# Kernel optimization log

Measured on AMD Instinct MI355X. Metric: run time of the kernel, lower is better.

The kernel has to match this reference:

```python
import jax, jax.numpy as jnp
import numpy as np

N0 = 4096
C = 128
DEPTH = 3
RATIO = 0.5
AVG_DEG = 32
BN_EPS = 1e-5


def setup_inputs() -> dict:
    key = jax.random.key(0)
    ks = jax.random.split(key, 6)
    x = jax.random.normal(ks[0], (N0, C), dtype=jnp.float32)
    # sparse symmetric adjacency (avg degree ~AVG_DEG), no self loops, dense layout
    mask = jax.random.bernoulli(ks[1], AVG_DEG / N0, (N0, N0)).astype(jnp.float32)
    adj = jnp.maximum(mask, mask.T) * (1.0 - jnp.eye(N0, dtype=jnp.float32))
    scale = 1.0 / np.sqrt(C)
    conv_w = jax.random.normal(ks[2], (2 * DEPTH + 1, C, C), dtype=jnp.float32) * scale
    conv_b = jax.random.normal(ks[3], (2 * DEPTH + 1, C), dtype=jnp.float32) * 0.01
    pool_w = jax.random.normal(ks[4], (DEPTH, C), dtype=jnp.float32)
    bn_g = jnp.ones((2 * DEPTH + 1, C), dtype=jnp.float32)
    bn_b = jnp.zeros((2 * DEPTH + 1, C), dtype=jnp.float32)
    return {"x": x, "adj": adj, "conv_w": conv_w, "conv_b": conv_b,
            "pool_w": pool_w, "bn_g": bn_g, "bn_b": bn_b}


def _gcn(x, A, W, b):
    # GCNConv(improved=True): A_hat = A + 2I, symmetric deg normalization
    n = A.shape[0]
    Ah = A + 2.0 * jnp.eye(n, dtype=A.dtype)
    deg = Ah.sum(axis=1)
    d_safe = jnp.where(deg > 0, deg, 1.0)
    dn = jnp.where(deg > 0, jax.lax.rsqrt(d_safe), 0.0)
    An = dn[:, None] * Ah * dn[None, :]
    return An @ (x @ W) + b


def _bn(x, g, b):
    # BatchNorm1d, training mode (biased variance)
    m = x.mean(axis=0)
    v = x.var(axis=0)
    return g * (x - m) * jax.lax.rsqrt(v + BN_EPS) + b


def _augment(A):
    # add_self_loops -> spspmm(A,A) -> remove_self_loops, done densely
    n = A.shape[0]
    I = jnp.eye(n, dtype=A.dtype)
    Aa = A + I
    return (Aa @ Aa) * (1.0 - I)


def _topk_pool(x, A, p):
    score = jnp.tanh((x @ p) / jnp.linalg.norm(p))
    k = int(np.ceil(RATIO * x.shape[0]))
    vals, perm = jax.lax.top_k(score, k)
    xn = x[perm] * vals[:, None]
    An = A[perm][:, perm]
    return xn, An, perm


def reference(x, adj, conv_w, conv_b, pool_w, bn_g, bn_b):
    x = x.astype(jnp.float32)
    x = _bn(jax.nn.relu(_gcn(x, adj, conv_w[0], conv_b[0])), bn_g[0], bn_b[0])
    xs, adjs, perms = [x], [adj], []
    A = adj
    for i in range(1, DEPTH + 1):
        A2 = _augment(A)
        x, A, perm = _topk_pool(x, A2, pool_w[i - 1])
        x = _bn(jax.nn.relu(_gcn(x, A, conv_w[i], conv_b[i])), bn_g[i], bn_b[i])
        if i < DEPTH:
            xs.append(x)
            adjs.append(A)
        perms.append(perm)
    for i in range(DEPTH):
        j = DEPTH - 1 - i
        res, Aj, perm = xs[j], adjs[j], perms[j]
        up = jnp.zeros_like(res).at[perm].set(x)
        x = res + up  # sum_res=True
        x = _gcn(x, Aj, conv_w[DEPTH + 1 + i], conv_b[DEPTH + 1 + i])
        if i < DEPTH - 1:
            x = jax.nn.relu(x)
        x = _bn(x, bn_g[DEPTH + 1 + i], bn_b[DEPTH + 1 + i])
    return x
```

## Files before the change

kernel.cpp:

```cpp
#include <hip/hip_runtime.h>
#include <cstdint>
#include <cstddef>

typedef __bf16 bf16;
typedef __bf16 bf16x8 __attribute__((ext_vector_type(8)));
typedef __bf16 bf16x4 __attribute__((ext_vector_type(4)));
typedef float floatx4 __attribute__((ext_vector_type(4)));
typedef int   intx4  __attribute__((ext_vector_type(4)));
typedef short shortx4 __attribute__((ext_vector_type(4)));
typedef char  cx8    __attribute__((ext_vector_type(8)));

#define GLD16(gp, lp) __builtin_amdgcn_global_load_lds( \
    (const __attribute__((address_space(1))) void*)(gp), \
    (__attribute__((address_space(3))) void*)(lp), 16, 0, 0)

#define FXS 16777216.0f
#define FXI 5.9604644775390625e-08

__global__ __launch_bounds__(256) void gemm_sym_i8(
    const char* __restrict__ R, short* __restrict__ Cs16, int* __restrict__ Cs32,
    int n , int kIters, int G, int pairs)
{
  __shared__ __align__(16) char As[128 * 64];
  __shared__ __align__(16) char Bs[128 * 64];

  const int pair = blockIdx.x;
  int rem = pair, bm = 0;
  while (rem >= G - bm) { rem -= G - bm; ++bm; }
  const int bn = bm + rem;
  const int m0 = bm * 128;
  const int n0 = bn * 128;

  const int t = threadIdx.x;
  const int w = t >> 6, l = t & 63;
  const int wr = w >> 1, wc = w & 1;
  const int lr = l & 15, q = l >> 4;
  const int k0base = blockIdx.y * kIters * 64;

  const char* Ab = R + (size_t)m0 * n + k0base;
  const char* Bb = R + (size_t)n0 * n + k0base;
  const int srow = t >> 2;
  const int schunk = (t & 3) * 16;

  intx4 acc[4][4];
#pragma unroll
  for (int i = 0; i < 4; ++i)
#pragma unroll
    for (int j = 0; j < 4; ++j) acc[i][j] = (intx4)0;

  for (int kb = 0; kb < kIters; ++kb) {
    const int k0 = kb * 64;
    __syncthreads();
    GLD16(Ab + (size_t)srow * n + k0 + schunk,        As + (size_t)t * 16);
    GLD16(Ab + (size_t)(srow + 64) * n + k0 + schunk, As + (size_t)(t + 256) * 16);
    GLD16(Bb + (size_t)srow * n + k0 + schunk,        Bs + (size_t)t * 16);
    GLD16(Bb + (size_t)(srow + 64) * n + k0 + schunk, Bs + (size_t)(t + 256) * 16);
    __syncthreads();

    intx4 af[4], bfr[4];
#pragma unroll
    for (int mi = 0; mi < 4; ++mi)
      af[mi] = *(const intx4*)&As[(wr * 64 + mi * 16 + lr) * 64 + q * 16];
#pragma unroll
    for (int ni = 0; ni < 4; ++ni)
      bfr[ni] = *(const intx4*)&Bs[(wc * 64 + ni * 16 + lr) * 64 + q * 16];
#pragma unroll
    for (int mi = 0; mi < 4; ++mi)
#pragma unroll
      for (int ni = 0; ni < 4; ++ni)
        acc[mi][ni] = __builtin_amdgcn_mfma_i32_16x16x64_i8(
            af[mi], bfr[ni], acc[mi][ni], 0, 0, 0);
  }

  const size_t so = ((size_t)blockIdx.y * pairs + pair) * 16384;
#pragma unroll
  for (int mi = 0; mi < 4; ++mi)
#pragma unroll
    for (int ni = 0; ni < 4; ++ni) {
      const int cl = wc * 64 + ni * 16 + lr;
      const int rb = wr * 64 + mi * 16 + q * 4;
#pragma unroll
      for (int r = 0; r < 4; ++r) {
        int v = acc[mi][ni][r];
        if (Cs16) Cs16[so + (size_t)(rb + r) * 128 + cl] = (short)v;
        else      Cs32[so + (size_t)(rb + r) * 128 + cl] = v;
      }
    }
}

__global__ void sym_post_i(const short* __restrict__ Cs16, const int* __restrict__ Cs32,
                           bf16* __restrict__ Abf, float* __restrict__ Af,
                           int k, int G, int pairs, int nz)
{
  int rem = blockIdx.x, bm = 0;
  while (rem >= G - bm) { rem -= G - bm; ++bm; }
  const int bn = bm + rem;
  const int t = threadIdx.x;
  const int i = t >> 1;
  const int jc = blockIdx.y * 8 + (t & 1) * 4;
  const int r = bm * 128 + i;
  const size_t sbase = (size_t)blockIdx.x * 16384 + (size_t)i * 128 + jc;

  int v[4] = {0, 0, 0, 0};
  for (int z = 0; z < nz; ++z) {
    const size_t off = sbase + (size_t)z * pairs * 16384;
    if (Cs16) {
      shortx4 a = *(const shortx4*)&Cs16[off];
#pragma unroll
      for (int e = 0; e < 4; ++e) v[e] += (int)a[e];
    } else {
      intx4 a = *(const intx4*)&Cs32[off];
#pragma unroll
      for (int e = 0; e < 4; ++e) v[e] += a[e];
    }
  }
  const int c0 = bn * 128 + jc;
#pragma unroll
  for (int e = 0; e < 4; ++e)
    if (c0 + e == r) v[e] = 0;

  if (Abf) {
    bf16x4 o;
#pragma unroll
    for (int e = 0; e < 4; ++e) o[e] = (bf16)(float)v[e];
    *(bf16x4*)&Abf[(size_t)r * k + c0] = o;
    if (bm != bn) {
#pragma unroll
      for (int e = 0; e < 4; ++e)
        Abf[(size_t)(c0 + e) * k + r] = o[e];
    }
  } else {
    floatx4 o;
#pragma unroll
    for (int e = 0; e < 4; ++e) o[e] = (float)v[e];
    *(floatx4*)&Af[(size_t)r * k + c0] = o;
    if (bm != bn) {
#pragma unroll
      for (int e = 0; e < 4; ++e)
        Af[(size_t)(c0 + e) * k + r] = o[e];
    }
  }
}

__global__ __launch_bounds__(256) void gemm_sym(
    const bf16* __restrict__ R, float* __restrict__ CsF,
    int n , int kIters, int G, int pairs)
{
  __shared__ __align__(16) bf16 As[128 * 32];
  __shared__ __align__(16) bf16 Bs[128 * 32];

  const int pair = blockIdx.x;
  int rem = pair, bm = 0;
  while (rem >= G - bm) { rem -= G - bm; ++bm; }
  const int bn = bm + rem;
  const int m0 = bm * 128;
  const int n0 = bn * 128;

  const int t = threadIdx.x;
  const int w = t >> 6, l = t & 63;
  const int wr = w >> 1, wc = w & 1;
  const int lr = l & 15, q = l >> 4;
  const int k0base = blockIdx.y * kIters * 32;

  const bf16* Ab = R + (size_t)m0 * n + k0base;
  const bf16* Bb = R + (size_t)n0 * n + k0base;
  const int srow = t >> 2;
  const int schunk = (t & 3) * 8;

  floatx4 acc[4][4];
#pragma unroll
  for (int i = 0; i < 4; ++i)
#pragma unroll
    for (int j = 0; j < 4; ++j) acc[i][j] = (floatx4)0.0f;

  for (int kb = 0; kb < kIters; ++kb) {
    const int k0 = kb * 32;
    __syncthreads();
    GLD16(Ab + (size_t)srow * n + k0 + schunk,        As + (size_t)t * 8);
    GLD16(Ab + (size_t)(srow + 64) * n + k0 + schunk, As + (size_t)(t + 256) * 8);
    GLD16(Bb + (size_t)srow * n + k0 + schunk,        Bs + (size_t)t * 8);
    GLD16(Bb + (size_t)(srow + 64) * n + k0 + schunk, Bs + (size_t)(t + 256) * 8);
    __syncthreads();

    bf16x8 af[4], bfr[4];
#pragma unroll
    for (int mi = 0; mi < 4; ++mi)
      af[mi] = *(const bf16x8*)&As[(wr * 64 + mi * 16 + lr) * 32 + q * 8];
#pragma unroll
    for (int ni = 0; ni < 4; ++ni)
      bfr[ni] = *(const bf16x8*)&Bs[(wc * 64 + ni * 16 + lr) * 32 + q * 8];
#pragma unroll
    for (int mi = 0; mi < 4; ++mi)
#pragma unroll
      for (int ni = 0; ni < 4; ++ni)
        acc[mi][ni] = __builtin_amdgcn_mfma_f32_16x16x32_bf16(
            af[mi], bfr[ni], acc[mi][ni], 0, 0, 0);
  }

  const size_t so = ((size_t)blockIdx.y * pairs + pair) * 16384;
#pragma unroll
  for (int mi = 0; mi < 4; ++mi)
#pragma unroll
    for (int ni = 0; ni < 4; ++ni) {
      const int cl = wc * 64 + ni * 16 + lr;
      const int rb = wr * 64 + mi * 16 + q * 4;
#pragma unroll
      for (int r = 0; r < 4; ++r)
        CsF[so + (size_t)(rb + r) * 128 + cl] = acc[mi][ni][r];
    }
}

__global__ void sym_post(const float* __restrict__ CsF, float* __restrict__ Af,
                         int k, int G, int pairs, int nz)
{
  int rem = blockIdx.x, bm = 0;
  while (rem >= G - bm) { rem -= G - bm; ++bm; }
  const int bn = bm + rem;
  const int t = threadIdx.x;
  const int i = t >> 1;
  const int jc = blockIdx.y * 8 + (t & 1) * 4;
  const int r = bm * 128 + i;
  const size_t sbase = (size_t)blockIdx.x * 16384 + (size_t)i * 128 + jc;

  float v[4] = {0.f, 0.f, 0.f, 0.f};
  for (int z = 0; z < nz; ++z) {
    const size_t off = sbase + (size_t)z * pairs * 16384;
    floatx4 a = *(const floatx4*)&CsF[off];
#pragma unroll
    for (int e = 0; e < 4; ++e) v[e] += a[e];
  }
  const int c0 = bn * 128 + jc;
  floatx4 o;
#pragma unroll
  for (int e = 0; e < 4; ++e) o[e] = (c0 + e == r) ? 0.0f : v[e];
  *(floatx4*)&Af[(size_t)r * k + c0] = o;
  if (bm != bn) {
#pragma unroll
    for (int e = 0; e < 4; ++e)
      Af[(size_t)(c0 + e) * k + r] = o[e];
  }
}

__global__ __launch_bounds__(256) void agg_sparse(
    const unsigned short* __restrict__ nbr, const int* __restrict__ deg,
    const float* __restrict__ Z, float* __restrict__ Y)
{
  const int r = blockIdx.x * 4 + (threadIdx.x >> 6);
  const int l = threadIdx.x & 63;
  const unsigned short* rn = nbr + (size_t)r * 256;
  const int d = deg[r];
  float a0 = 0.f, a1 = 0.f;
  int i = 0;
  for (; i + 4 <= d; i += 4) {
    const int c0 = rn[i], c1 = rn[i + 1], c2 = rn[i + 2], c3 = rn[i + 3];
    float2 v0 = *(const float2*)(Z + (size_t)c0 * 128 + l * 2);
    float2 v1 = *(const float2*)(Z + (size_t)c1 * 128 + l * 2);
    float2 v2 = *(const float2*)(Z + (size_t)c2 * 128 + l * 2);
    float2 v3 = *(const float2*)(Z + (size_t)c3 * 128 + l * 2);
    a0 += v0.x; a1 += v0.y;
    a0 += v1.x; a1 += v1.y;
    a0 += v2.x; a1 += v2.y;
    a0 += v3.x; a1 += v3.y;
  }
  for (; i < d; ++i) {
    const int c = rn[i];
    float2 v = *(const float2*)(Z + (size_t)c * 128 + l * 2);
    a0 += v.x; a1 += v.y;
  }
  *(float2*)(Y + (size_t)r * 128 + l * 2) = make_float2(a0, a1);
}

template <int NP>
__global__ __launch_bounds__(256) void agg_bf(
    const bf16* __restrict__ A, int lda,
    const bf16* __restrict__ Zh, const bf16* __restrict__ Zm, const bf16* __restrict__ Zl,
    int ldz, float* __restrict__ Y, int kIters)
{
  __shared__ __align__(16) bf16 As[64 * 32];
  __shared__ __align__(16) bf16 Zs[NP][128 * 32];

  const int t = threadIdx.x;
  const int w = t >> 6, l = t & 63;
  const int wr = w >> 1, wc = w & 1;
  const int lr = l & 15, q = l >> 4;
  const int m0 = blockIdx.x * 64;
  const int k0base = blockIdx.y * kIters * 32;

  const int srow = t >> 2;
  const int schunk = (t & 3) * 8;

  floatx4 acc[2][4];
#pragma unroll
  for (int i = 0; i < 2; ++i)
#pragma unroll
    for (int j = 0; j < 4; ++j) acc[i][j] = (floatx4)0.0f;

  for (int kb = 0; kb < kIters; ++kb) {
    const int k0 = k0base + kb * 32;
    __syncthreads();
    GLD16(A + (size_t)(m0 + srow) * lda + k0 + schunk, As + (size_t)t * 8);
    GLD16(Zh + (size_t)srow * ldz + k0 + schunk,        Zs[0] + (size_t)t * 8);
    GLD16(Zh + (size_t)(srow + 64) * ldz + k0 + schunk, Zs[0] + (size_t)(t + 256) * 8);
    GLD16(Zm + (size_t)srow * ldz + k0 + schunk,        Zs[1] + (size_t)t * 8);
    GLD16(Zm + (size_t)(srow + 64) * ldz + k0 + schunk, Zs[1] + (size_t)(t + 256) * 8);
    if (NP > 2) {
      GLD16(Zl + (size_t)srow * ldz + k0 + schunk,        Zs[2] + (size_t)t * 8);
      GLD16(Zl + (size_t)(srow + 64) * ldz + k0 + schunk, Zs[2] + (size_t)(t + 256) * 8);
    }
    __syncthreads();

    bf16x8 af[2], bz[NP][4];
#pragma unroll
    for (int mi = 0; mi < 2; ++mi)
      af[mi] = *(const bf16x8*)&As[(wr * 32 + mi * 16 + lr) * 32 + q * 8];
#pragma unroll
    for (int s = 0; s < NP; ++s)
#pragma unroll
      for (int ni = 0; ni < 4; ++ni)
        bz[s][ni] = *(const bf16x8*)&Zs[s][(wc * 64 + ni * 16 + lr) * 32 + q * 8];
#pragma unroll
    for (int s = 0; s < NP; ++s)
#pragma unroll
      for (int mi = 0; mi < 2; ++mi)
#pragma unroll
        for (int ni = 0; ni < 4; ++ni)
          acc[mi][ni] = __builtin_amdgcn_mfma_f32_16x16x32_bf16(
              af[mi], bz[s][ni], acc[mi][ni], 0, 0, 0);
  }

  const size_t zoff = (size_t)blockIdx.y * lda;
#pragma unroll
  for (int mi = 0; mi < 2; ++mi)
#pragma unroll
    for (int ni = 0; ni < 4; ++ni) {
      const int col = wc * 64 + ni * 16 + lr;
      const int rowb = m0 + wr * 32 + mi * 16 + q * 4;
#pragma unroll
      for (int r = 0; r < 4; ++r)
        Y[(zoff + rowb + r) * 128 + col] = acc[mi][ni][r];
    }
}

template <int NP>
__global__ __launch_bounds__(256) void agg_split(
    const float* __restrict__ A, int lda,
    const bf16* __restrict__ Zh, const bf16* __restrict__ Zm, const bf16* __restrict__ Zl,
    int ldz, float* __restrict__ Y, int kIters, int aTwo)
{
  __shared__ __align__(16) bf16 Ahs[64 * 32];
  __shared__ __align__(16) bf16 Als[64 * 32];
  __shared__ __align__(16) bf16 Zs[NP][128 * 32];

  const int t = threadIdx.x;
  const int w = t >> 6, l = t & 63;
  const int wr = w >> 1, wc = w & 1;
  const int lr = l & 15, q = l >> 4;
  const int m0 = blockIdx.x * 64;
  const int k0base = blockIdx.y * kIters * 32;

  const int arow = t >> 2;
  const int acol = (t & 3) * 8;
  const int srow = t >> 2;
  const int schunk = (t & 3) * 8;

  floatx4 acc[2][4];
#pragma unroll
  for (int i = 0; i < 2; ++i)
#pragma unroll
    for (int j = 0; j < 4; ++j) acc[i][j] = (floatx4)0.0f;

  for (int kb = 0; kb < kIters; ++kb) {
    const int k0 = k0base + kb * 32;
    const float* asrc = A + (size_t)(m0 + arow) * lda + k0 + acol;
    floatx4 av[2];
#pragma unroll
    for (int i = 0; i < 2; ++i) av[i] = *(const floatx4*)(asrc + i * 4);

    __syncthreads();
    GLD16(Zh + (size_t)srow * ldz + k0 + schunk,        Zs[0] + (size_t)t * 8);
    GLD16(Zh + (size_t)(srow + 64) * ldz + k0 + schunk, Zs[0] + (size_t)(t + 256) * 8);
    GLD16(Zm + (size_t)srow * ldz + k0 + schunk,        Zs[1] + (size_t)t * 8);
    GLD16(Zm + (size_t)(srow + 64) * ldz + k0 + schunk, Zs[1] + (size_t)(t + 256) * 8);
    if (NP > 2) {
      GLD16(Zl + (size_t)srow * ldz + k0 + schunk,        Zs[2] + (size_t)t * 8);
      GLD16(Zl + (size_t)(srow + 64) * ldz + k0 + schunk, Zs[2] + (size_t)(t + 256) * 8);
    }

    bf16x4 ah[2], alo[2];
    const int grow = m0 + arow;
#pragma unroll
    for (int i = 0; i < 8; ++i) {
      float v = av[i >> 2][i & 3];
      if (k0 + acol + i == grow) v = 0.0f;
      bf16 h = (bf16)v;
      ah[i >> 2][i & 3] = h;
      alo[i >> 2][i & 3] = (bf16)(v - (float)h);
    }
    const int sbase = arow * 32 + acol;
    *(bf16x4*)&Ahs[sbase] = ah[0]; *(bf16x4*)&Ahs[sbase + 4] = ah[1];
    if (aTwo) { *(bf16x4*)&Als[sbase] = alo[0]; *(bf16x4*)&Als[sbase + 4] = alo[1]; }
    __syncthreads();

    bf16x8 afh[2], afl[2], bz[NP][4];
#pragma unroll
    for (int mi = 0; mi < 2; ++mi)
      afh[mi] = *(const bf16x8*)&Ahs[(wr * 32 + mi * 16 + lr) * 32 + q * 8];
#pragma unroll
    for (int s = 0; s < NP; ++s)
#pragma unroll
      for (int ni = 0; ni < 4; ++ni)
        bz[s][ni] = *(const bf16x8*)&Zs[s][(wc * 64 + ni * 16 + lr) * 32 + q * 8];
#pragma unroll
    for (int s = 0; s < NP; ++s)
#pragma unroll
      for (int mi = 0; mi < 2; ++mi)
#pragma unroll
        for (int ni = 0; ni < 4; ++ni)
          acc[mi][ni] = __builtin_amdgcn_mfma_f32_16x16x32_bf16(
              afh[mi], bz[s][ni], acc[mi][ni], 0, 0, 0);
    if (aTwo) {
#pragma unroll
      for (int mi = 0; mi < 2; ++mi)
        afl[mi] = *(const bf16x8*)&Als[(wr * 32 + mi * 16 + lr) * 32 + q * 8];
      constexpr int NL = (NP > 2) ? 2 : 1;
#pragma unroll
      for (int s = 0; s < NL; ++s)
#pragma unroll
        for (int mi = 0; mi < 2; ++mi)
#pragma unroll
          for (int ni = 0; ni < 4; ++ni)
            acc[mi][ni] = __builtin_amdgcn_mfma_f32_16x16x32_bf16(
                afl[mi], bz[s][ni], acc[mi][ni], 0, 0, 0);
    }
  }

  const size_t zoff = (size_t)blockIdx.y * lda;
#pragma unroll
  for (int mi = 0; mi < 2; ++mi)
#pragma unroll
    for (int ni = 0; ni < 4; ++ni) {
      const int col = wc * 64 + ni * 16 + lr;
      const int rowb = m0 + wr * 32 + mi * 16 + q * 4;
#pragma unroll
      for (int r = 0; r < 4; ++r)
        Y[(zoff + rowb + r) * 128 + col] = acc[mi][ni][r];
    }
}

template <int FULL>
__global__ __launch_bounds__(256) void xw_split(
    const float* __restrict__ X, const int* __restrict__ perm,
    const float* __restrict__ vals,
    const float* __restrict__ up, const int* __restrict__ inv,
    const long long* __restrict__ statsP, const float* __restrict__ gP,
    const float* __restrict__ bP, float nP,
    const bf16* __restrict__ Wh, const bf16* __restrict__ Wm, const bf16* __restrict__ Wl,
    const float* __restrict__ dnv, float* __restrict__ Z,
    bf16* __restrict__ Zht, bf16* __restrict__ Zmt, bf16* __restrict__ Zlt, int ldz,
    long long* __restrict__ stats)
{
  __shared__ __align__(16) bf16 Xs[3][128 * 32];
  __shared__ __align__(16) bf16 Ws[3][128 * 32];
  __shared__ float scU[128], offU[128];

  const int t = threadIdx.x;
  if (blockIdx.x == 0) stats[t] = 0;

  const int w = t >> 6, l = t & 63;
  const int wr = w >> 1, wc = w & 1;
  const int lr = l & 15, q = l >> 4;
  const int r0 = blockIdx.x * 128;

  const int srow = t >> 1;
  const int soff = (t & 1) * 16;
  const int sbase = srow * 32 + soff;

  if (statsP) {
    if (t < 128) {
      float sm = (float)((double)statsP[t] * FXI);
      float sq = (float)((double)statsP[128 + t] * FXI);
      float m = sm / nP;
      float var = sq / nP - m * m;
      float sc = gP[t] / sqrtf(var + 1e-5f);
      scU[t] = sc;
      offU[t] = bP[t] - m * sc;
    }
    __syncthreads();
  }

  const int row = r0 + srow;
  int grow = row;
  float scale = 1.0f;
  if (perm) { grow = perm[row]; scale = vals[row]; }
  const float* xrow = X + (size_t)grow * 128;
  const float* uprow = nullptr;
  if (up) { int j = inv[row]; if (j >= 0) uprow = up + (size_t)j * 128; }

  floatx4 acc[4][4];
#pragma unroll
  for (int i = 0; i < 4; ++i)
#pragma unroll
    for (int j = 0; j < 4; ++j) acc[i][j] = (floatx4)0.0f;

  const bf16* wsrc[3] = {Wh, Wm, Wl};

  for (int ks = 0; ks < 4; ++ks) {
    const int k0 = ks * 32;
    float xv[16];
#pragma unroll
    for (int i = 0; i < 16; i += 4) {
      floatx4 tmp = *(const floatx4*)(xrow + k0 + soff + i);
      if (uprow) {
        floatx4 u = *(const floatx4*)(uprow + k0 + soff + i);
        if (statsP) {
#pragma unroll
          for (int j = 0; j < 4; ++j) {
            const int c = k0 + soff + i + j;
            u[j] = scU[c] * u[j] + offU[c];
          }
        }
        tmp += u;
      }
      xv[i] = tmp[0] * scale; xv[i + 1] = tmp[1] * scale;
      xv[i + 2] = tmp[2] * scale; xv[i + 3] = tmp[3] * scale;
    }
    bf16x8 wv[3][2];
#pragma unroll
    for (int s = 0; s < 3; ++s) {
      const bf16* ws = wsrc[s] + (size_t)srow * 128 + k0 + soff;
      wv[s][0] = *(const bf16x8*)ws;
      wv[s][1] = *(const bf16x8*)(ws + 8);
    }
    bf16x8 vh[2], vm[2], vl[2];
#pragma unroll
    for (int i = 0; i < 16; ++i) {
      float v = xv[i];
      bf16 h = (bf16)v; float r1 = v - (float)h;
      bf16 m = (bf16)r1; float r2 = r1 - (float)m;
      vh[i >> 3][i & 7] = h; vm[i >> 3][i & 7] = m; vl[i >> 3][i & 7] = (bf16)r2;
    }
    __syncthreads();
    *(bf16x8*)&Xs[0][sbase] = vh[0]; *(bf16x8*)&Xs[0][sbase + 8] = vh[1];
    *(bf16x8*)&Xs[1][sbase] = vm[0]; *(bf16x8*)&Xs[1][sbase + 8] = vm[1];
    *(bf16x8*)&Xs[2][sbase] = vl[0]; *(bf16x8*)&Xs[2][sbase + 8] = vl[1];
#pragma unroll
    for (int s = 0; s < 3; ++s) {
      *(bf16x8*)&Ws[s][sbase] = wv[s][0];
      *(bf16x8*)&Ws[s][sbase + 8] = wv[s][1];
    }
    __syncthreads();

    bf16x8 af[3][4], bfg[3][4];
#pragma unroll
    for (int s = 0; s < 3; ++s) {
#pragma unroll
      for (int mi = 0; mi < 4; ++mi)
        af[s][mi] = *(const bf16x8*)&Xs[s][(wr * 64 + mi * 16 + lr) * 32 + q * 8];
#pragma unroll
      for (int ni = 0; ni < 4; ++ni)
        bfg[s][ni] = *(const bf16x8*)&Ws[s][(wc * 64 + ni * 16 + lr) * 32 + q * 8];
    }
    constexpr int NT = FULL ? 6 : 3;
    constexpr int sa[6] = {0, 0, 1, 1, 0, 2};
    constexpr int sb[6] = {0, 1, 0, 1, 2, 0};
#pragma unroll
    for (int p = 0; p < NT; ++p)
#pragma unroll
      for (int mi = 0; mi < 4; ++mi)
#pragma unroll
        for (int ni = 0; ni < 4; ++ni)
          acc[mi][ni] = __builtin_amdgcn_mfma_f32_16x16x32_bf16(
              af[sa[p]][mi], bfg[sb[p]][ni], acc[mi][ni], 0, 0, 0);
  }

#pragma unroll
  for (int mi = 0; mi < 4; ++mi) {
    const int rowb = r0 + wr * 64 + mi * 16 + q * 4;
    float dnr[4];
#pragma unroll
    for (int r = 0; r < 4; ++r) dnr[r] = dnv[rowb + r];
#pragma unroll
    for (int ni = 0; ni < 4; ++ni) {
      const int col = wc * 64 + ni * 16 + lr;
      bf16x4 h4, m4, l4;
#pragma unroll
      for (int r = 0; r < 4; ++r) {
        float v = dnr[r] * acc[mi][ni][r];
        Z[(size_t)(rowb + r) * 128 + col] = v;
        bf16 h = (bf16)v; float r1 = v - (float)h;
        bf16 m = (bf16)r1; float r2 = r1 - (float)m;
        h4[r] = h; m4[r] = m; l4[r] = (bf16)r2;
      }
      if (Zht) {
        *(bf16x4*)&Zht[(size_t)col * ldz + rowb] = h4;
        *(bf16x4*)&Zmt[(size_t)col * ldz + rowb] = m4;
        if (FULL) *(bf16x4*)&Zlt[(size_t)col * ldz + rowb] = l4;
      }
    }
  }
}

__global__ void prep_all(const float* __restrict__ adj, bf16* __restrict__ ah,
                         float* __restrict__ dn, int n,
                         unsigned short* __restrict__ nbr, int* __restrict__ deg,
                         const float* __restrict__ W, bf16* __restrict__ Wh,
                         bf16* __restrict__ Wm, bf16* __restrict__ Wl,
                         const float* __restrict__ pw, float* __restrict__ invp) {
  const int bid = blockIdx.x;
  const int t = threadIdx.x;
  __shared__ int wsum4[4];
  __shared__ float red[128];
  if (bid < 4096) {
    const int r = bid;
    const float* arow = adj + (size_t)r * n;
    bf16* orow = ah + (size_t)r * n;
    const int base = t * 16;
    floatx4 buf[4];
#pragma unroll
    for (int i = 0; i < 4; ++i) buf[i] = *(const floatx4*)(arow + base + i * 4);
    int cnt = 0;
#pragma unroll
    for (int i = 0; i < 4; ++i) {
      bf16x4 o;
#pragma unroll
      for (int e = 0; e < 4; ++e) {
        float x = (base + i * 4 + e == r) ? 0.0f : buf[i][e];
        buf[i][e] = x;
        cnt += (x != 0.0f) ? 1 : 0;
        o[e] = (bf16)x;
      }
      *(bf16x4*)&orow[base + i * 4] = o;
    }
    const int lane = t & 63, wid = t >> 6;
    int vc = cnt;
#pragma unroll
    for (int off = 1; off < 64; off <<= 1) {
      int u = __shfl_up(vc, off, 64);
      if (lane >= off) vc += u;
    }
    if (lane == 63) wsum4[wid] = vc;
    __syncthreads();
    int add = 0;
    for (int wi = 0; wi < wid; ++wi) add += wsum4[wi];
    int o = vc + add - cnt;
    const int total = wsum4[0] + wsum4[1] + wsum4[2] + wsum4[3];
    unsigned short* rn = nbr + (size_t)r * 256;
#pragma unroll
    for (int i = 0; i < 4; ++i)
#pragma unroll
      for (int e = 0; e < 4; ++e)
        if (buf[i][e] != 0.0f) {
          if (o < 256) rn[o] = (unsigned short)(base + i * 4 + e);
          ++o;
        }
    if (t == 0) {
      deg[r] = total < 256 ? total : 256;
      dn[r] = 1.0f / sqrtf((float)total + 2.0f);
    }
  } else if (bid < 4544) {
    int idx = (bid - 4096) * 256 + t;
    int l = idx >> 14, rem = idx & 16383, c = rem >> 7, k = rem & 127;
    float v = W[(l << 14) + (k << 7) + c];
    bf16 h = (bf16)v; float r1 = v - (float)h;
    bf16 m = (bf16)r1; float r2 = r1 - (float)m;
    Wh[idx] = h; Wm[idx] = m; Wl[idx] = (bf16)r2;
  } else {
    if (t < 128) {
      for (int l = 0; l < 3; ++l) {
        float v = pw[l * 128 + t];
        red[t] = v * v; __syncthreads();
        for (int off = 64; off; off >>= 1) {
          if (t < off) red[t] += red[t + off];
          __syncthreads();
        }
        if (t == 0) invp[l] = 1.0f / sqrtf(red[0]);
        __syncthreads();
      }
    }
  }
}

__global__ void dn_rows_bf(const bf16* __restrict__ A, int lda, float* __restrict__ dn,
                           int n) {
  int r = blockIdx.x, t = threadIdx.x;
  const bf16* row = A + (size_t)r * lda;
  float sum = 0.f;
  for (int c4 = t * 4; c4 < n; c4 += 1024) {
    bf16x4 v = *(const bf16x4*)&row[c4];
#pragma unroll
    for (int e = 0; e < 4; ++e) sum += (float)v[e];
  }
  __shared__ float red[256];
  red[t] = sum; __syncthreads();
  for (int off = 128; off; off >>= 1) {
    if (t < off) red[t] += red[t + off];
    __syncthreads();
  }
  if (t == 0) dn[r] = 1.0f / sqrtf(red[0] + 2.0f);
}

__global__ void dn_rows(const float* __restrict__ A, int lda, float* __restrict__ dn,
                        int n) {
  int r = blockIdx.x, t = threadIdx.x;
  const float* row = A + (size_t)r * lda;
  float sum = 0.f;
  for (int c = t; c < n; c += 256)
    if (c != r) sum += row[c];
  __shared__ float red[256];
  red[t] = sum; __syncthreads();
  for (int off = 128; off; off >>= 1) {
    if (t < off) red[t] += red[t + off];
    __syncthreads();
  }
  if (t == 0) dn[r] = 1.0f / sqrtf(red[0] + 2.0f);
}

__device__ inline unsigned f2u(float f) {
  unsigned u = __float_as_uint(f);
  return (u & 0x80000000u) ? ~u : (u | 0x80000000u);
}
__global__ __launch_bounds__(1024) void select_kernel(
    const float* __restrict__ s, int n, int k,
    int* __restrict__ perm, float* __restrict__ vals, int* __restrict__ inv)
{
  __shared__ int hist[256];
  __shared__ unsigned sh_prefix;
  __shared__ int sh_krem;
  __shared__ float sh_thr;
  __shared__ int wsum[16];
  __shared__ int wgs[16], wes[16];
  const int t = threadIdx.x;
  const int lane = t & 63;
  const int wid = t >> 6;
  if (t == 0) { sh_prefix = 0; sh_krem = k; }

  for (int round = 0; round < 4; ++round) {
    const int shift = 24 - 8 * round;
    if (t < 256) hist[t] = 0;
    __syncthreads();
    const unsigned pref = sh_prefix;
    const int krem = sh_krem;
    for (int i = t; i < n; i += 1024) {
      unsigned u = f2u(s[i]);
      if (round == 0 || (u >> (shift + 8)) == pref)
        atomicAdd(&hist[(u >> shift) & 255], 1);
    }
    __syncthreads();
    int v = 0, own = 0;
    if (t < 256) {
      own = hist[255 - t];
      v = own;
#pragma unroll
      for (int off = 1; off < 64; off <<= 1) {
        int u = __shfl_up(v, off, 64);
        if (lane >= off) v += u;
      }
      if (lane == 63) wsum[wid] = v;
    }
    __syncthreads();
    if (t < 256) {
      int add = 0;
      for (int wi = 0; wi < wid; ++wi) add += wsum[wi];
      v += add;
      const int prev = v - own;
      if (v >= krem && prev < krem) {
        sh_prefix = (pref << 8) | (unsigned)(255 - t);
        sh_krem = krem - prev;
      }
    }
    __syncthreads();
  }
  if (t == 0) {
    unsigned u = sh_prefix;
    sh_thr = (u & 0x80000000u) ? __uint_as_float(u & 0x7fffffffu)
                               : __uint_as_float(~u);
  }
  for (int i = t; i < n; i += 1024) inv[i] = -1;
  __syncthreads();

  const float thr = sh_thr;
  const int chunk = n >> 10;
  const int beg = t * chunk;
  int g = 0, e = 0;
  for (int i = 0; i < chunk; ++i) {
    float v = s[beg + i];
    g += (v > thr); e += (v == thr);
  }
  int vg = g, ve = e;
#pragma unroll
  for (int off = 1; off < 64; off <<= 1) {
    int ug = __shfl_up(vg, off, 64);
    int ue = __shfl_up(ve, off, 64);
    if (lane >= off) { vg += ug; ve += ue; }
  }
  if (lane == 63) { wgs[wid] = vg; wes[wid] = ve; }
  __syncthreads();
  int ag = 0, ae = 0;
  for (int wi = 0; wi < wid; ++wi) { ag += wgs[wi]; ae += wes[wi]; }
  int total_gt = 0;
#pragma unroll
  for (int wi = 0; wi < 16; ++wi) total_gt += wgs[wi];
  int pg = vg + ag - g;
  int pe = ve + ae - e;
  const int need = k - total_gt;
  for (int i = 0; i < chunk; ++i) {
    float v = s[beg + i];
    if (v > thr) {
      if (pg < k) { perm[pg] = beg + i; vals[pg] = v; inv[beg + i] = pg; }
      ++pg;
    } else if (v == thr) {
      if (pe < need && total_gt + pe < k) {
        perm[total_gt + pe] = beg + i; vals[total_gt + pe] = v;
        inv[beg + i] = total_gt + pe;
      }
      ++pe;
    }
  }
}

__global__ void gather_i8(const bf16* __restrict__ src, int lda,
                          const int* __restrict__ perm, char* __restrict__ R, int n) {
  int j = blockIdx.x, t = threadIdx.x;
  int r = perm[j];
  const bf16* s = src + (size_t)r * lda;
  char* o = R + (size_t)j * n;
  for (int c = t * 8; c < n; c += 2048) {
    bf16x8 v = *(const bf16x8*)&s[c];
    cx8 ob;
#pragma unroll
    for (int e = 0; e < 8; ++e)
      ob[e] = (c + e == r) ? (char)1 : (char)(float)v[e];
    *(cx8*)&o[c] = ob;
  }
}

__global__ void gather_f32(const float* __restrict__ src, int lda,
                           const int* __restrict__ perm, bf16* __restrict__ R, int n) {
  int j = blockIdx.x, t = threadIdx.x;
  int r = perm[j];
  const float* s = src + (size_t)r * lda;
  bf16* o = R + (size_t)j * n;
  for (int c4 = t * 4; c4 < n; c4 += 1024) {
    floatx4 v = *(const floatx4*)(s + c4);
    bf16x4 ob;
#pragma unroll
    for (int e = 0; e < 4; ++e)
      ob[e] = (c4 + e == r) ? (bf16)1.0f : (bf16)v[e];
    *(bf16x4*)&o[c4] = ob;
  }
}

__global__ void gcn_post(const float* Ys, const float* __restrict__ Zf,
                         const float* __restrict__ dn, const float* __restrict__ bias,
                         long long* __restrict__ stats, int relu,
                         float* hout, int nr, int nz) {
  int c = threadIdx.x;
  int r0 = blockIdx.x * 4;
  float b = bias[c];
  float s = 0.f, qq = 0.f;
  for (int i = 0; i < 4; ++i) {
    int r = r0 + i;
    float a = 0.f;
    for (int z = 0; z < nz; ++z)
      a += Ys[((size_t)z * nr + r) * 128 + c];
    float v = dn[r] * (a + 2.0f * Zf[(size_t)r * 128 + c]) + b;
    if (relu) v = fmaxf(v, 0.f);
    hout[(size_t)r * 128 + c] = v;
    s += v; qq += v * v;
  }
  atomicAdd((unsigned long long*)&stats[c],
            (unsigned long long)(long long)llrintf(s * FXS));
  atomicAdd((unsigned long long*)&stats[128 + c],
            (unsigned long long)(long long)llrintf(qq * FXS));
}

__global__ void bn_apply(const float* __restrict__ H, const long long* __restrict__ stats,
                         const float* __restrict__ g, const float* __restrict__ b,
                         int n, float* __restrict__ xout,
                         const float* __restrict__ pw, const float* __restrict__ invp,
                         float* __restrict__ scores) {
  int r = blockIdx.x, c = threadIdx.x;
  float sm = (float)((double)stats[c] * FXI);
  float sq = (float)((double)stats[128 + c] * FXI);
  float m = sm / n;
  float var = sq / n - m * m;
  float sc = g[c] / sqrtf(var + 1e-5f);
  float off = b[c] - m * sc;
  float v = sc * H[(size_t)r * 128 + c] + off;
  xout[(size_t)r * 128 + c] = v;
  if (pw) {
    __shared__ float red[128];
    red[c] = v * pw[c]; __syncthreads();
    for (int o = 64; o; o >>= 1) {
      if (c < o) red[c] += red[c + o];
      __syncthreads();
    }
    if (c == 0) scores[r] = tanhf(red[0] * invp[0]);
  }
}

extern "C" void kernel_launch(void* const* d_in, const int* in_sizes, int n_in,
                              void* d_out, int out_size, void* d_ws, size_t ws_size,
                              hipStream_t stream) {
  const float* x_in   = (const float*)d_in[0];
  const float* adj    = (const float*)d_in[1];
  const float* conv_w = (const float*)d_in[2];
  const float* conv_b = (const float*)d_in[3];
  const float* pool_w = (const float*)d_in[4];
  const float* bn_g   = (const float*)d_in[5];
  const float* bn_b   = (const float*)d_in[6];
  float* out = (float*)d_out;
  (void)in_sizes; (void)n_in; (void)out_size; (void)ws_size;

  char* p = (char*)d_ws;
  auto alloc = [&](size_t bytes) -> void* {
    void* r = (void*)p;
    p += (bytes + 255) & ~(size_t)255;
    return r;
  };
  bf16*  Ah0bf = (bf16*)alloc(4096ull * 4096 * 2);
  bf16*  A1bf  = (bf16*)alloc(2048ull * 2048 * 2);
  float* A2f   = (float*)alloc(1024ull * 1024 * 4);
  float* A3f   = (float*)alloc(512ull * 512 * 4);
  char*  Rbuf  = (char*)alloc(2048ull * 4096 * 2);
  void*  Cs    = alloc(40ull << 20);
  float* Z     = (float*)alloc(4096ull * 128 * 4);
  bf16*  Zht   = (bf16*)alloc(128ull * 4096 * 2);
  bf16*  Zmt   = (bf16*)alloc(128ull * 4096 * 2);
  bf16*  Zlt   = (bf16*)alloc(128ull * 4096 * 2);
  float* Agg   = (float*)alloc(8ull * 2048 * 128 * 4);
  float* res0  = (float*)alloc(4096ull * 128 * 4);
  float* res1  = (float*)alloc(2048ull * 128 * 4);
  float* res2  = (float*)alloc(1024ull * 128 * 4);
  float* xb0   = (float*)alloc(512ull * 128 * 4);
  float* xb1   = (float*)alloc(1024ull * 128 * 4);
  float* xb2   = (float*)alloc(2048ull * 128 * 4);
  bf16*  Wh    = (bf16*)alloc(7ull * 16384 * 2);
  bf16*  Wm    = (bf16*)alloc(7ull * 16384 * 2);
  bf16*  Wl    = (bf16*)alloc(7ull * 16384 * 2);
  unsigned short* nbr = (unsigned short*)alloc(4096ull * 256 * 2 + 1024);
  int*   deg   = (int*)alloc(4096 * 4);
  float* scores = (float*)alloc(4096 * 4);
  int*   perm0 = (int*)alloc(2048 * 4);
  int*   perm1 = (int*)alloc(1024 * 4);
  int*   perm2 = (int*)alloc(512 * 4);
  int*   inv0  = (int*)alloc(4096 * 4);
  int*   inv1  = (int*)alloc(2048 * 4);
  int*   inv2  = (int*)alloc(1024 * 4);
  float* vals0 = (float*)alloc(2048 * 4);
  float* vals1 = (float*)alloc(1024 * 4);
  float* vals2 = (float*)alloc(512 * 4);
  float* dn0   = (float*)alloc(4096 * 4);
  float* dn1   = (float*)alloc(2048 * 4);
  float* dn2   = (float*)alloc(1024 * 4);
  float* dn3   = (float*)alloc(512 * 4);
  float* invp  = (float*)alloc(256);
  long long* stats = (long long*)alloc(7ull * 256 * 8);

  auto gcn = [&](int nr, const bf16* Abf, const float* Af32,
                 const unsigned short* nbrp, const float* dnv,
                 int layer, const float* xsrc, const int* perm, const float* vals,
                 const float* up, const int* inv, float* xout, int relu, int aTwo,
                 const float* pw, const float* ip, int full,
                 const long long* statsP, const float* gP, const float* bPv, float nP,
                 int doBn) {
    long long* st = stats + layer * 256;
    bf16* zht = nbrp ? nullptr : Zht;
    bf16* zmt = nbrp ? nullptr : Zmt;
    bf16* zlt = nbrp ? nullptr : Zlt;
    if (full)
      xw_split<1><<<nr / 128, 256, 0, stream>>>(
          xsrc, perm, vals, up, inv, statsP, gP, bPv, nP,
          Wh + layer * 16384, Wm + layer * 16384, Wl + layer * 16384, dnv,
          Z, zht, zmt, zlt, nr, st);
    else
      xw_split<0><<<nr / 128, 256, 0, stream>>>(
          xsrc, perm, vals, up, inv, statsP, gP, bPv, nP,
          Wh + layer * 16384, Wm + layer * 16384, Wl + layer * 16384, dnv,
          Z, zht, zmt, zlt, nr, st);
    int nz;
    if (nbrp) {
      agg_sparse<<<nr / 4, 256, 0, stream>>>(nbrp, deg, Z, Agg);
      nz = 1;
    } else if (Abf) {
      if (full)
        agg_bf<3><<<dim3(nr / 64, 8), 256, 0, stream>>>(
            Abf, nr, Zht, Zmt, Zlt, nr, Agg, nr / 256);
      else
        agg_bf<2><<<dim3(nr / 64, 8), 256, 0, stream>>>(
            Abf, nr, Zht, Zmt, Zlt, nr, Agg, nr / 256);
      nz = 8;
    } else {
      if (full)
        agg_split<3><<<dim3(nr / 64, 8), 256, 0, stream>>>(
            Af32, nr, Zht, Zmt, Zlt, nr, Agg, nr / 256, aTwo);
      else
        agg_split<2><<<dim3(nr / 64, 8), 256, 0, stream>>>(
            Af32, nr, Zht, Zmt, Zlt, nr, Agg, nr / 256, aTwo);
      nz = 8;
    }
    gcn_post<<<nr / 4, 128, 0, stream>>>(Agg, Z, dnv, conv_b + layer * 128, st, relu,
                                         doBn ? Agg : xout, nr, nz);
    if (doBn)
      bn_apply<<<nr, 128, 0, stream>>>(Agg, st, bn_g + layer * 128, bn_b + layer * 128,
                                       nr, xout, pw, ip, scores);
  };

  auto pool = [&](int n, const bf16* srcBf, const float* srcF32,
                  bf16* outBf, float* outF32, float* dnNew,
                  int* perm, float* vals, int* inv, int splitZ, int mode) {
    int k = n / 2, G = k / 128, pairs = G * (G + 1) / 2;
    select_kernel<<<1, 1024, 0, stream>>>(scores, n, k, perm, vals, inv);
    if (mode <= 1) {
      gather_i8<<<k, 256, 0, stream>>>(srcBf, n, perm, Rbuf, n);
      gemm_sym_i8<<<dim3(pairs, splitZ), 256, 0, stream>>>(
          Rbuf, mode == 0 ? (short*)Cs : nullptr, mode == 0 ? nullptr : (int*)Cs,
          n, n / (splitZ * 64), G, pairs);
      sym_post_i<<<dim3(pairs, 16), 256, 0, stream>>>(
          mode == 0 ? (const short*)Cs : nullptr, mode == 0 ? nullptr : (const int*)Cs,
          outBf, outF32, k, G, pairs, splitZ);
    } else {
      gather_f32<<<k, 256, 0, stream>>>(srcF32, n, perm, (bf16*)Rbuf, n);
      gemm_sym<<<dim3(pairs, splitZ), 256, 0, stream>>>(
          (const bf16*)Rbuf, (float*)Cs, n, n / (splitZ * 32), G, pairs);
      sym_post<<<dim3(pairs, 16), 256, 0, stream>>>(
          (const float*)Cs, outF32, k, G, pairs, splitZ);
    }
    if (outBf) dn_rows_bf<<<k, 256, 0, stream>>>(outBf, k, dnNew, k);
    else       dn_rows<<<k, 256, 0, stream>>>(outF32, k, dnNew, k);
  };

  prep_all<<<4545, 256, 0, stream>>>(adj, Ah0bf, dn0, 4096, nbr, deg,
                                     conv_w, Wh, Wm, Wl, pool_w, invp);

  gcn(4096, nullptr, nullptr, nbr, dn0, 0, x_in, nullptr, nullptr, nullptr, nullptr,
      res0, 1, 0, pool_w + 0, invp + 0, 1, nullptr, nullptr, nullptr, 1.0f, 1);
  pool(4096, Ah0bf, nullptr, A1bf, nullptr, dn1, perm0, vals0, inv0, 4, 0);
  gcn(2048, A1bf, nullptr, nullptr, dn1, 1, res0, perm0, vals0, nullptr, nullptr,
      res1, 1, 0, pool_w + 128, invp + 1, 1, nullptr, nullptr, nullptr, 1.0f, 1);
  pool(2048, A1bf, nullptr, nullptr, A2f, dn2, perm1, vals1, inv1, 8, 1);
  gcn(1024, nullptr, A2f, nullptr, dn2, 2, res1, perm1, vals1, nullptr, nullptr,
      res2, 1, 1, pool_w + 256, invp + 2, 1, nullptr, nullptr, nullptr, 1.0f, 1);
  pool(1024, nullptr, A2f, nullptr, A3f, dn3, perm2, vals2, inv2, 8, 2);
  gcn(512, nullptr, A3f, nullptr, dn3, 3, res2, perm2, vals2, nullptr, nullptr,
      xb0, 1, 1, nullptr, nullptr, 0, nullptr, nullptr, nullptr, 1.0f, 0);

  gcn(1024, nullptr, A2f, nullptr, dn2, 4, res2, nullptr, nullptr, xb0, inv2,
      xb1, 1, 1, nullptr, nullptr, 0,
      stats + 3 * 256, bn_g + 3 * 128, bn_b + 3 * 128, 512.0f, 0);
  gcn(2048, A1bf, nullptr, nullptr, dn1, 5, res1, nullptr, nullptr, xb1, inv1,
      xb2, 1, 0, nullptr, nullptr, 0,
      stats + 4 * 256, bn_g + 4 * 128, bn_b + 4 * 128, 1024.0f, 0);
  gcn(4096, nullptr, nullptr, nbr, dn0, 6, res0, nullptr, nullptr, xb2, inv0,
      out, 0, 0, nullptr, nullptr, 0,
      stats + 5 * 256, bn_g + 5 * 128, bn_b + 5 * 128, 2048.0f, 1);
}
```

Baseline: 533.6 us.

## Fuse degree sums into sym_post via atomics and reduce agg splits with fixed-point atomics

Removes the separate dn_rows kernels by accumulating row degree sums with float atomics in the symmetric post-processing kernels, zeroing the accumulators in the gather kernels. The aggregation kernels now reduce their K-split partials directly into a zeroed int64 fixed-point buffer with 64-bit atomics instead of writing 8 partial slabs that gcn_post then sums. The aim is fewer kernel launches and less partial-buffer traffic, at the cost of heavy atomic contention and added conversion work. Fixed-point atomics keep the sum deterministic, while the float degree atomics are exact only because the values are small integers.

```diff
diff --git a/kernel.cpp b/kernel.cpp
--- a/kernel.cpp
+++ b/kernel.cpp
@@ -90,6 +90,7 @@
 
 __global__ void sym_post_i(const short* __restrict__ Cs16, const int* __restrict__ Cs32,
                            bf16* __restrict__ Abf, float* __restrict__ Af,
+                           float* __restrict__ dnS,
                            int k, int G, int pairs, int nz)
 {
   int rem = blockIdx.x, bm = 0;
@@ -119,6 +120,9 @@
   for (int e = 0; e < 4; ++e)
     if (c0 + e == r) v[e] = 0;
 
+  const int rs = v[0] + v[1] + v[2] + v[3];
+  atomicAdd(&dnS[r], (float)rs);
+
   if (Abf) {
     bf16x4 o;
 #pragma unroll
@@ -126,8 +130,10 @@
     *(bf16x4*)&Abf[(size_t)r * k + c0] = o;
     if (bm != bn) {
 #pragma unroll
-      for (int e = 0; e < 4; ++e)
+      for (int e = 0; e < 4; ++e) {
         Abf[(size_t)(c0 + e) * k + r] = o[e];
+        atomicAdd(&dnS[c0 + e], (float)v[e]);
+      }
     }
   } else {
     floatx4 o;
@@ -136,8 +142,10 @@
     *(floatx4*)&Af[(size_t)r * k + c0] = o;
     if (bm != bn) {
 #pragma unroll
-      for (int e = 0; e < 4; ++e)
+      for (int e = 0; e < 4; ++e) {
         Af[(size_t)(c0 + e) * k + r] = o[e];
+        atomicAdd(&dnS[c0 + e], (float)v[e]);
+      }
     }
   }
 }
@@ -211,6 +219,7 @@
 }
 
 __global__ void sym_post(const float* __restrict__ CsF, float* __restrict__ Af,
+                         float* __restrict__ dnS,
                          int k, int G, int pairs, int nz)
 {
   int rem = blockIdx.x, bm = 0;
@@ -233,11 +242,14 @@
   floatx4 o;
 #pragma unroll
   for (int e = 0; e < 4; ++e) o[e] = (c0 + e == r) ? 0.0f : v[e];
+  atomicAdd(&dnS[r], o[0] + o[1] + o[2] + o[3]);
   *(floatx4*)&Af[(size_t)r * k + c0] = o;
   if (bm != bn) {
 #pragma unroll
-    for (int e = 0; e < 4; ++e)
+    for (int e = 0; e < 4; ++e) {
       Af[(size_t)(c0 + e) * k + r] = o[e];
+      atomicAdd(&dnS[c0 + e], o[e]);
+    }
   }
 }
 
@@ -274,7 +286,7 @@
 __global__ __launch_bounds__(256) void agg_bf(
     const bf16* __restrict__ A, int lda,
     const bf16* __restrict__ Zh, const bf16* __restrict__ Zm, const bf16* __restrict__ Zl,
-    int ldz, float* __restrict__ Y, int kIters)
+    int ldz, long long* __restrict__ YI, int kIters)
 {
   __shared__ __align__(16) bf16 As[64 * 32];
   __shared__ __align__(16) bf16 Zs[NP][128 * 32];
@@ -328,7 +340,6 @@
               af[mi], bz[s][ni], acc[mi][ni], 0, 0, 0);
   }
 
-  const size_t zoff = (size_t)blockIdx.y * lda;
 #pragma unroll
   for (int mi = 0; mi < 2; ++mi)
 #pragma unroll
@@ -337,7 +348,8 @@
       const int rowb = m0 + wr * 32 + mi * 16 + q * 4;
 #pragma unroll
       for (int r = 0; r < 4; ++r)
-        Y[(zoff + rowb + r) * 128 + col] = acc[mi][ni][r];
+        atomicAdd((unsigned long long*)&YI[(size_t)(rowb + r) * 128 + col],
+                  (unsigned long long)(long long)llrintf(acc[mi][ni][r] * FXS));
     }
 }
 
@@ -345,7 +357,7 @@
 __global__ __launch_bounds__(256) void agg_split(
     const float* __restrict__ A, int lda,
     const bf16* __restrict__ Zh, const bf16* __restrict__ Zm, const bf16* __restrict__ Zl,
-    int ldz, float* __restrict__ Y, int kIters, int aTwo)
+    int ldz, long long* __restrict__ YI, int kIters, int aTwo)
 {
   __shared__ __align__(16) bf16 Ahs[64 * 32];
   __shared__ __align__(16) bf16 Als[64 * 32];
@@ -434,7 +446,6 @@
     }
   }
 
-  const size_t zoff = (size_t)blockIdx.y * lda;
 #pragma unroll
   for (int mi = 0; mi < 2; ++mi)
 #pragma unroll
@@ -443,7 +454,8 @@
       const int rowb = m0 + wr * 32 + mi * 16 + q * 4;
 #pragma unroll
       for (int r = 0; r < 4; ++r)
-        Y[(zoff + rowb + r) * 128 + col] = acc[mi][ni][r];
+        atomicAdd((unsigned long long*)&YI[(size_t)(rowb + r) * 128 + col],
+                  (unsigned long long)(long long)llrintf(acc[mi][ni][r] * FXS));
     }
 }
 
@@ -457,7 +469,7 @@
     const bf16* __restrict__ Wh, const bf16* __restrict__ Wm, const bf16* __restrict__ Wl,
     const float* __restrict__ dnv, float* __restrict__ Z,
     bf16* __restrict__ Zht, bf16* __restrict__ Zmt, bf16* __restrict__ Zlt, int ldz,
-    long long* __restrict__ stats)
+    long long* __restrict__ AggI, long long* __restrict__ stats)
 {
   __shared__ __align__(16) bf16 Xs[3][128 * 32];
   __shared__ __align__(16) bf16 Ws[3][128 * 32];
@@ -578,7 +590,7 @@
     const int rowb = r0 + wr * 64 + mi * 16 + q * 4;
     float dnr[4];
 #pragma unroll
-    for (int r = 0; r < 4; ++r) dnr[r] = dnv[rowb + r];
+    for (int r = 0; r < 4; ++r) dnr[r] = 1.0f / sqrtf(dnv[rowb + r] + 2.0f);
 #pragma unroll
     for (int ni = 0; ni < 4; ++ni) {
       const int col = wc * 64 + ni * 16 + lr;
@@ -592,6 +604,9 @@
         h4[r] = h; m4[r] = m; l4[r] = (bf16)r2;
       }
       if (Zht) {
+#pragma unroll
+        for (int r = 0; r < 4; ++r)
+          AggI[(size_t)(rowb + r) * 128 + col] = 0;
         *(bf16x4*)&Zht[(size_t)col * ldz + rowb] = h4;
         *(bf16x4*)&Zmt[(size_t)col * ldz + rowb] = m4;
         if (FULL) *(bf16x4*)&Zlt[(size_t)col * ldz + rowb] = l4;
@@ -655,7 +670,7 @@
         }
     if (t == 0) {
       deg[r] = total < 256 ? total : 256;
-      dn[r] = 1.0f / sqrtf((float)total + 2.0f);
+      dn[r] = (float)total;
     }
   } else if (bid < 4544) {
     int idx = (bid - 4096) * 256 + t;
@@ -680,41 +695,6 @@
   }
 }
 
-__global__ void dn_rows_bf(const bf16* __restrict__ A, int lda, float* __restrict__ dn,
-                           int n) {
-  int r = blockIdx.x, t = threadIdx.x;
-  const bf16* row = A + (size_t)r * lda;
-  float sum = 0.f;
-  for (int c4 = t * 4; c4 < n; c4 += 1024) {
-    bf16x4 v = *(const bf16x4*)&row[c4];
-#pragma unroll
-    for (int e = 0; e < 4; ++e) sum += (float)v[e];
-  }
-  __shared__ float red[256];
-  red[t] = sum; __syncthreads();
-  for (int off = 128; off; off >>= 1) {
-    if (t < off) red[t] += red[t + off];
-    __syncthreads();
-  }
-  if (t == 0) dn[r] = 1.0f / sqrtf(red[0] + 2.0f);
-}
-
-__global__ void dn_rows(const float* __restrict__ A, int lda, float* __restrict__ dn,
-                        int n) {
-  int r = blockIdx.x, t = threadIdx.x;
-  const float* row = A + (size_t)r * lda;
-  float sum = 0.f;
-  for (int c = t; c < n; c += 256)
-    if (c != r) sum += row[c];
-  __shared__ float red[256];
-  red[t] = sum; __syncthreads();
-  for (int off = 128; off; off >>= 1) {
-    if (t < off) red[t] += red[t + off];
-    __syncthreads();
-  }
-  if (t == 0) dn[r] = 1.0f / sqrtf(red[0] + 2.0f);
-}
-
 __device__ inline unsigned f2u(float f) {
   unsigned u = __float_as_uint(f);
   return (u & 0x80000000u) ? ~u : (u | 0x80000000u);
@@ -819,9 +799,11 @@
 }
 
 __global__ void gather_i8(const bf16* __restrict__ src, int lda,
-                          const int* __restrict__ perm, char* __restrict__ R, int n) {
+                          const int* __restrict__ perm, char* __restrict__ R, int n,
+                          float* __restrict__ dnz) {
   int j = blockIdx.x, t = threadIdx.x;
   int r = perm[j];
+  if (t == 0) dnz[j] = 0.0f;
   const bf16* s = src + (size_t)r * lda;
   char* o = R + (size_t)j * n;
   for (int c = t * 8; c < n; c += 2048) {
@@ -835,9 +817,11 @@
 }
 
 __global__ void gather_f32(const float* __restrict__ src, int lda,
-                           const int* __restrict__ perm, bf16* __restrict__ R, int n) {
+                           const int* __restrict__ perm, bf16* __restrict__ R, int n,
+                           float* __restrict__ dnz) {
   int j = blockIdx.x, t = threadIdx.x;
   int r = perm[j];
+  if (t == 0) dnz[j] = 0.0f;
   const float* s = src + (size_t)r * lda;
   bf16* o = R + (size_t)j * n;
   for (int c4 = t * 4; c4 < n; c4 += 1024) {
@@ -850,20 +834,21 @@
   }
 }
 
-__global__ void gcn_post(const float* Ys, const float* __restrict__ Zf,
+__global__ void gcn_post(const long long* __restrict__ YsI, const float* YsF,
+                         const float* __restrict__ Zf,
                          const float* __restrict__ dn, const float* __restrict__ bias,
                          long long* __restrict__ stats, int relu,
-                         float* hout, int nr, int nz) {
+                         float* hout) {
   int c = threadIdx.x;
   int r0 = blockIdx.x * 4;
   float b = bias[c];
   float s = 0.f, qq = 0.f;
   for (int i = 0; i < 4; ++i) {
     int r = r0 + i;
-    float a = 0.f;
-    for (int z = 0; z < nz; ++z)
-      a += Ys[((size_t)z * nr + r) * 128 + c];
-    float v = dn[r] * (a + 2.0f * Zf[(size_t)r * 128 + c]) + b;
+    float a = YsI ? (float)((double)YsI[(size_t)r * 128 + c] * FXI)
+                  : YsF[(size_t)r * 128 + c];
+    float d = 1.0f / sqrtf(dn[r] + 2.0f);
+    float v = d * (a + 2.0f * Zf[(size_t)r * 128 + c]) + b;
     if (relu) v = fmaxf(v, 0.f);
     hout[(size_t)r * 128 + c] = v;
     s += v; qq += v * v;
@@ -928,7 +913,8 @@
   bf16*  Zht   = (bf16*)alloc(128ull * 4096 * 2);
   bf16*  Zmt   = (bf16*)alloc(128ull * 4096 * 2);
   bf16*  Zlt   = (bf16*)alloc(128ull * 4096 * 2);
-  float* Agg   = (float*)alloc(8ull * 2048 * 128 * 4);
+  float* Agg   = (float*)alloc(4096ull * 128 * 4);
+  long long* AggI = (long long*)alloc(4096ull * 128 * 8);
   float* res0  = (float*)alloc(4096ull * 128 * 4);
   float* res1  = (float*)alloc(2048ull * 128 * 4);
   float* res2  = (float*)alloc(1024ull * 128 * 4);
@@ -972,35 +958,34 @@
       xw_split<1><<<nr / 128, 256, 0, stream>>>(
           xsrc, perm, vals, up, inv, statsP, gP, bPv, nP,
           Wh + layer * 16384, Wm + layer * 16384, Wl + layer * 16384, dnv,
-          Z, zht, zmt, zlt, nr, st);
+          Z, zht, zmt, zlt, nr, AggI, st);
     else
       xw_split<0><<<nr / 128, 256, 0, stream>>>(
           xsrc, perm, vals, up, inv, statsP, gP, bPv, nP,
           Wh + layer * 16384, Wm + layer * 16384, Wl + layer * 16384, dnv,
-          Z, zht, zmt, zlt, nr, st);
-    int nz;
+          Z, zht, zmt, zlt, nr, AggI, st);
+    const long long* aggI = nullptr;
     if (nbrp) {
       agg_sparse<<<nr / 4, 256, 0, stream>>>(nbrp, deg, Z, Agg);
-      nz = 1;
     } else if (Abf) {
       if (full)
         agg_bf<3><<<dim3(nr / 64, 8), 256, 0, stream>>>(
-            Abf, nr, Zht, Zmt, Zlt, nr, Agg, nr / 256);
+            Abf, nr, Zht, Zmt, Zlt, nr, AggI, nr / 256);
       else
         agg_bf<2><<<dim3(nr / 64, 8), 256, 0, stream>>>(
-            Abf, nr, Zht, Zmt, Zlt, nr, Agg, nr / 256);
-      nz = 8;
+            Abf, nr, Zht, Zmt, Zlt, nr, AggI, nr / 256);
+      aggI = AggI;
     } else {
       if (full)
         agg_split<3><<<dim3(nr / 64, 8), 256, 0, stream>>>(
-            Af32, nr, Zht, Zmt, Zlt, nr, Agg, nr / 256, aTwo);
+            Af32, nr, Zht, Zmt, Zlt, nr, AggI, nr / 256, aTwo);
       else
         agg_split<2><<<dim3(nr / 64, 8), 256, 0, stream>>>(
-            Af32, nr, Zht, Zmt, Zlt, nr, Agg, nr / 256, aTwo);
-      nz = 8;
-    }
-    gcn_post<<<nr / 4, 128, 0, stream>>>(Agg, Z, dnv, conv_b + layer * 128, st, relu,
-                                         doBn ? Agg : xout, nr, nz);
+            Af32, nr, Zht, Zmt, Zlt, nr, AggI, nr / 256, aTwo);
+      aggI = AggI;
+    }
+    gcn_post<<<nr / 4, 128, 0, stream>>>(aggI, Agg, Z, dnv, conv_b + layer * 128,
+                                         st, relu, doBn ? Agg : xout);
     if (doBn)
       bn_apply<<<nr, 128, 0, stream>>>(Agg, st, bn_g + layer * 128, bn_b + layer * 128,
                                        nr, xout, pw, ip, scores);
@@ -1012,22 +997,20 @@
     int k = n / 2, G = k / 128, pairs = G * (G + 1) / 2;
     select_kernel<<<1, 1024, 0, stream>>>(scores, n, k, perm, vals, inv);
     if (mode <= 1) {
-      gather_i8<<<k, 256, 0, stream>>>(srcBf, n, perm, Rbuf, n);
+      gather_i8<<<k, 256, 0, stream>>>(srcBf, n, perm, Rbuf, n, dnNew);
       gemm_sym_i8<<<dim3(pairs, splitZ), 256, 0, stream>>>(
           Rbuf, mode == 0 ? (short*)Cs : nullptr, mode == 0 ? nullptr : (int*)Cs,
           n, n / (splitZ * 64), G, pairs);
       sym_post_i<<<dim3(pairs, 16), 256, 0, stream>>>(
           mode == 0 ? (const short*)Cs : nullptr, mode == 0 ? nullptr : (const int*)Cs,
-          outBf, outF32, k, G, pairs, splitZ);
+          outBf, outF32, dnNew, k, G, pairs, splitZ);
     } else {
-      gather_f32<<<k, 256, 0, stream>>>(srcF32, n, perm, (bf16*)Rbuf, n);
+      gather_f32<<<k, 256, 0, stream>>>(srcF32, n, perm, (bf16*)Rbuf, n, dnNew);
       gemm_sym<<<dim3(pairs, splitZ), 256, 0, stream>>>(
           (const bf16*)Rbuf, (float*)Cs, n, n / (splitZ * 32), G, pairs);
       sym_post<<<dim3(pairs, 16), 256, 0, stream>>>(
-          (const float*)Cs, outF32, k, G, pairs, splitZ);
-    }
-    if (outBf) dn_rows_bf<<<k, 256, 0, stream>>>(outBf, k, dnNew, k);
-    else       dn_rows<<<k, 256, 0, stream>>>(outF32, k, dnNew, k);
+          (const float*)Cs, outF32, dnNew, k, G, pairs, splitZ);
+    }
   };
 
   prep_all<<<4545, 256, 0, stream>>>(adj, Ah0bf, dn0, 4096, nbr, deg,
```

Result: slower. 1.404 ms (+163.1%).
